# Performance work log

Hardware: AMD Instinct MI355X
Metric: run time of the kernel (lower is better)

The kernel has to match this reference:

```python
import jax, jax.numpy as jnp
import numpy as np

T, B, D, H = 2048, 64, 256, 512

def setup_inputs() -> dict:
    key = jax.random.key(0)
    ks = jax.random.split(key, 4)
    s = 1.0 / np.sqrt(D + H)  # nn.Linear default uniform scale approximated with normal*s
    return {
        "x": jax.random.normal(ks[0], (T, B, D), dtype=jnp.float32),
        "h0": jnp.zeros((B, H), dtype=jnp.float32),
        "Wz": jax.random.normal(ks[1], (D + H, H), dtype=jnp.float32) * s,
        "bz": jnp.zeros((H,), dtype=jnp.float32),
        "Wr": jax.random.normal(ks[2], (D + H, H), dtype=jnp.float32) * s,
        "br": jnp.zeros((H,), dtype=jnp.float32),
        "Wh": jax.random.normal(ks[3], (D + H, H), dtype=jnp.float32) * s,
        "bh": jnp.zeros((H,), dtype=jnp.float32),
    }

def reference(x, h0, Wz, bz, Wr, br, Wh, bh):
    """GRU over time: x [T,B,D], h0 [B,H]; returns hidden history [T,B,H]."""
    def step(h, xt):
        xh = jnp.concatenate([xt, h], axis=-1)          # [B, D+H]
        z = jax.nn.sigmoid(xh @ Wz + bz)                # update gate
        r = jax.nn.sigmoid(xh @ Wr + br)                # reset gate
        xrh = jnp.concatenate([xt, r * h], axis=-1)     # [B, D+H]
        h_tilde = jnp.tanh(xrh @ Wh + bh)               # candidate state
        h_new = (1.0 - z) * h + z * h_tilde
        return h_new, h_new
    _, hist = jax.lax.scan(step, h0, x)
    return hist
```

## Files before the change

### kernel.cpp

```cpp
#include <hip/hip_runtime.h>
#include <stdint.h>


#define T_STEPS 2048
#define B_SZ    64
#define D_SZ    256
#define H_SZ    512
#define NGROUP  4
#define NWG     64
#define MB      16

typedef __attribute__((ext_vector_type(8))) short  short8;
typedef __attribute__((ext_vector_type(4))) float  f32x4;
typedef unsigned long long u64;

__device__ __forceinline__ unsigned short f2bf(float v) {
  uint32_t u = __float_as_uint(v);
  return (unsigned short)((u + 0x7fffu + ((u >> 16) & 1u)) >> 16);
}
__device__ __forceinline__ float bf2f(unsigned short h) {
  return __uint_as_float(((uint32_t)h) << 16);
}
__device__ __forceinline__ void splitf(float v, short& hi, short& lo) {
  unsigned short h = f2bf(v);
  hi = (short)h;
  lo = (short)f2bf(v - bf2f(h));
}
__device__ __forceinline__ uint32_t packf(float v) {
  unsigned short h = f2bf(v);
  unsigned short l = f2bf(v - bf2f(h));
  return ((uint32_t)h << 16) | (uint32_t)l;
}
__device__ __forceinline__ float unpackf(uint32_t p) {
  return __uint_as_float(p & 0xffff0000u) + __uint_as_float(p << 16);
}

__device__ __forceinline__ uint32_t aload32(const uint32_t* p) {
  return __hip_atomic_load(p, __ATOMIC_RELAXED, __HIP_MEMORY_SCOPE_AGENT);
}
__device__ __forceinline__ u64 aload64(const uint32_t* p) {
  return __hip_atomic_load((const unsigned long long*)p, __ATOMIC_RELAXED,
                           __HIP_MEMORY_SCOPE_AGENT);
}
__device__ __forceinline__ void astore32(uint32_t* p, uint32_t v) {
  __hip_atomic_store(p, v, __ATOMIC_RELAXED, __HIP_MEMORY_SCOPE_AGENT);
}

__device__ __forceinline__ void lds_barrier() {
  asm volatile("s_waitcnt lgkmcnt(0)" ::: "memory");
  __builtin_amdgcn_s_barrier();
}

__device__ __forceinline__ void poll_flags(const uint32_t* fl, uint32_t tgt,
                                           int lane, int& cap) {
  int guard = 0;
  for (;;) {
    uint32_t v = aload32(fl + (lane & 31));
    if (__all((int)(v >= tgt))) break;
    if (++guard > cap) { cap = 256; break; }
    __builtin_amdgcn_s_sleep(1);
  }
}

__global__ void __launch_bounds__(256, 1)
gru_roles(const float* __restrict__ x, const float* __restrict__ h0,
          const float* __restrict__ Wz, const float* __restrict__ bz,
          const float* __restrict__ Wr, const float* __restrict__ br,
          const float* __restrict__ Wh, const float* __restrict__ bh,
          float* __restrict__ out,
          uint32_t* rh_flg, uint32_t* h_flg,
          uint32_t* h_pk, uint32_t* rh_pk, uint32_t* z_pk)
{
  __shared__ float partTa[16 * 64];
  __shared__ float partTb[16 * 64];

  const int tid  = threadIdx.x;
  const int wv   = tid >> 6;
  const int lane = tid & 63;
  const int blk  = blockIdx.x;
  const int g    = blk >> 6;
  const int wid  = blk & 63;
  const int m0   = g * MB;
  const bool isGate = (wid < 32);

  const int n     = lane & 15;
  const int kq    = lane >> 4;
  const int bfrag = m0 + n;
  const int m2    = kq * 4 + wv;
  const int n2    = n;
  const int b2    = m0 + m2;

  uint32_t* frh = rh_flg + g * 32;
  uint32_t* fh  = h_flg  + g * 32;

  int lch[6];
  lch[0] = 2 * wv; lch[1] = 2 * wv + 1;
  #pragma unroll
  for (int l = 2; l < 6; ++l) lch[l] = 8 + 4 * wv + (l - 2);

  int cap = 1 << 20;

  if (isGate) {
    const int c1  = wid * 16;
    const int col = c1 + n;

    short8 wzh[6], wzl[6], wrh_[6], wrl_[6];
    #pragma unroll
    for (int l = 0; l < 6; ++l) {
      #pragma unroll
      for (int j = 0; j < 8; ++j) {
        const int k = lch[l] * 32 + kq * 8 + j;
        short hi, lo;
        splitf(Wz[(size_t)k * H_SZ + col], hi, lo); wzh[l][j] = hi; wzl[l][j] = lo;
        splitf(Wr[(size_t)k * H_SZ + col], hi, lo); wrh_[l][j] = hi; wrl_[l][j] = lo;
      }
    }
    const float bzv = bz[col];
    const float brv = br[col];

    #pragma unroll 1
    for (int t = 0; t < T_STEPS; ++t) {
      f32x4 aZ = {0.f, 0.f, 0.f, 0.f};
      f32x4 aR = {0.f, 0.f, 0.f, 0.f};
      #pragma unroll
      for (int l = 0; l < 2; ++l) {
        const float* xp = x + ((size_t)t * B_SZ + bfrag) * D_SZ + lch[l] * 32 + kq * 8;
        float4 f0 = *(const float4*)xp;
        float4 f1 = *(const float4*)(xp + 4);
        float f[8] = {f0.x, f0.y, f0.z, f0.w, f1.x, f1.y, f1.z, f1.w};
        short8 xh, xl;
        #pragma unroll
        for (int j = 0; j < 8; ++j) { short hi, lo; splitf(f[j], hi, lo); xh[j] = hi; xl[j] = lo; }
        aZ = __builtin_amdgcn_mfma_f32_16x16x32_bf16(xh, wzh[l], aZ, 0, 0, 0);
        aZ = __builtin_amdgcn_mfma_f32_16x16x32_bf16(xl, wzh[l], aZ, 0, 0, 0);
        aZ = __builtin_amdgcn_mfma_f32_16x16x32_bf16(xh, wzl[l], aZ, 0, 0, 0);
        aR = __builtin_amdgcn_mfma_f32_16x16x32_bf16(xh, wrh_[l], aR, 0, 0, 0);
        aR = __builtin_amdgcn_mfma_f32_16x16x32_bf16(xl, wrh_[l], aR, 0, 0, 0);
        aR = __builtin_amdgcn_mfma_f32_16x16x32_bf16(xh, wrl_[l], aR, 0, 0, 0);
      }

      float hval;
      if (t > 0) {
        poll_flags(fh, (uint32_t)t, lane, cap);
        uint32_t hv = aload32(h_pk + (size_t)b2 * H_SZ + c1 + n2);
        #pragma unroll
        for (int l = 2; l < 6; ++l) {
          const int kh = (lch[l] - 8) * 32 + kq * 8;
          const uint32_t* hp = h_pk + (size_t)bfrag * H_SZ + kh;
          u64 q0 = aload64(hp),     q1 = aload64(hp + 2);
          u64 q2 = aload64(hp + 4), q3 = aload64(hp + 6);
          uint32_t u[8] = {(uint32_t)q0, (uint32_t)(q0 >> 32), (uint32_t)q1, (uint32_t)(q1 >> 32),
                           (uint32_t)q2, (uint32_t)(q2 >> 32), (uint32_t)q3, (uint32_t)(q3 >> 32)};
          short8 hh, hl;
          #pragma unroll
          for (int j = 0; j < 8; ++j) { hh[j] = (short)(u[j] >> 16); hl[j] = (short)(u[j] & 0xffffu); }
          aZ = __builtin_amdgcn_mfma_f32_16x16x32_bf16(hh, wzh[l], aZ, 0, 0, 0);
          aZ = __builtin_amdgcn_mfma_f32_16x16x32_bf16(hl, wzh[l], aZ, 0, 0, 0);
          aZ = __builtin_amdgcn_mfma_f32_16x16x32_bf16(hh, wzl[l], aZ, 0, 0, 0);
          aR = __builtin_amdgcn_mfma_f32_16x16x32_bf16(hh, wrh_[l], aR, 0, 0, 0);
          aR = __builtin_amdgcn_mfma_f32_16x16x32_bf16(hl, wrh_[l], aR, 0, 0, 0);
          aR = __builtin_amdgcn_mfma_f32_16x16x32_bf16(hh, wrl_[l], aR, 0, 0, 0);
        }
        hval = unpackf(hv);
      } else {
        hval = h0[(size_t)b2 * H_SZ + c1 + n2];
        #pragma unroll
        for (int l = 2; l < 6; ++l) {
          const int kh = (lch[l] - 8) * 32 + kq * 8;
          const float* hp = h0 + (size_t)bfrag * H_SZ + kh;
          float4 f0 = *(const float4*)hp;
          float4 f1 = *(const float4*)(hp + 4);
          float f[8] = {f0.x, f0.y, f0.z, f0.w, f1.x, f1.y, f1.z, f1.w};
          short8 hh, hl;
          #pragma unroll
          for (int j = 0; j < 8; ++j) { short hi, lo; splitf(f[j], hi, lo); hh[j] = hi; hl[j] = lo; }
          aZ = __builtin_amdgcn_mfma_f32_16x16x32_bf16(hh, wzh[l], aZ, 0, 0, 0);
          aZ = __builtin_amdgcn_mfma_f32_16x16x32_bf16(hl, wzh[l], aZ, 0, 0, 0);
          aZ = __builtin_amdgcn_mfma_f32_16x16x32_bf16(hh, wzl[l], aZ, 0, 0, 0);
          aR = __builtin_amdgcn_mfma_f32_16x16x32_bf16(hh, wrh_[l], aR, 0, 0, 0);
          aR = __builtin_amdgcn_mfma_f32_16x16x32_bf16(hl, wrh_[l], aR, 0, 0, 0);
          aR = __builtin_amdgcn_mfma_f32_16x16x32_bf16(hh, wrl_[l], aR, 0, 0, 0);
        }
      }

      #pragma unroll
      for (int r = 0; r < 4; ++r) {
        partTa[(wv * 4 + r) * 64 + lane] = aZ[r];
        partTb[(wv * 4 + r) * 64 + lane] = aR[r];
      }
      lds_barrier();
      {
        float sZ = partTa[(0 + wv) * 64 + lane] + partTa[(4 + wv) * 64 + lane]
                 + partTa[(8 + wv) * 64 + lane] + partTa[(12 + wv) * 64 + lane] + bzv;
        float sR = partTb[(0 + wv) * 64 + lane] + partTb[(4 + wv) * 64 + lane]
                 + partTb[(8 + wv) * 64 + lane] + partTb[(12 + wv) * 64 + lane] + brv;
        float zg = 1.f / (1.f + __expf(-sZ));
        float rg = 1.f / (1.f + __expf(-sR));
        astore32(z_pk  + (size_t)b2 * H_SZ + c1 + n2, __float_as_uint(zg));
        astore32(rh_pk + (size_t)b2 * H_SZ + c1 + n2, packf(rg * hval));
      }
      asm volatile("s_waitcnt vmcnt(0)" ::: "memory");
      lds_barrier();
      if (tid == 0) astore32(frh + wid, (uint32_t)(t + 1));
    }
  } else {
    const int c2  = (wid - 32) * 16;
    const int col = c2 + n;

    short8 whh_[6], whl_[6];
    #pragma unroll
    for (int l = 0; l < 6; ++l) {
      #pragma unroll
      for (int j = 0; j < 8; ++j) {
        const int k = lch[l] * 32 + kq * 8 + j;
        short hi, lo;
        splitf(Wh[(size_t)k * H_SZ + col], hi, lo); whh_[l][j] = hi; whl_[l][j] = lo;
      }
    }
    const float bhv = bh[col];

    float hreg = h0[(size_t)b2 * H_SZ + c2 + n2];

    #pragma unroll 1
    for (int t = 0; t < T_STEPS; ++t) {
      f32x4 acc = {0.f, 0.f, 0.f, 0.f};
      #pragma unroll
      for (int l = 0; l < 2; ++l) {
        const float* xp = x + ((size_t)t * B_SZ + bfrag) * D_SZ + lch[l] * 32 + kq * 8;
        float4 f0 = *(const float4*)xp;
        float4 f1 = *(const float4*)(xp + 4);
        float f[8] = {f0.x, f0.y, f0.z, f0.w, f1.x, f1.y, f1.z, f1.w};
        short8 xh, xl;
        #pragma unroll
        for (int j = 0; j < 8; ++j) { short hi, lo; splitf(f[j], hi, lo); xh[j] = hi; xl[j] = lo; }
        acc = __builtin_amdgcn_mfma_f32_16x16x32_bf16(xh, whh_[l], acc, 0, 0, 0);
        acc = __builtin_amdgcn_mfma_f32_16x16x32_bf16(xl, whh_[l], acc, 0, 0, 0);
        acc = __builtin_amdgcn_mfma_f32_16x16x32_bf16(xh, whl_[l], acc, 0, 0, 0);
      }

      poll_flags(frh, (uint32_t)(t + 1), lane, cap);
      uint32_t zu = aload32(z_pk + (size_t)b2 * H_SZ + c2 + n2);
      #pragma unroll
      for (int l = 2; l < 6; ++l) {
        const int kh = (lch[l] - 8) * 32 + kq * 8;
        const uint32_t* rp = rh_pk + (size_t)bfrag * H_SZ + kh;
        u64 q0 = aload64(rp),     q1 = aload64(rp + 2);
        u64 q2 = aload64(rp + 4), q3 = aload64(rp + 6);
        uint32_t u[8] = {(uint32_t)q0, (uint32_t)(q0 >> 32), (uint32_t)q1, (uint32_t)(q1 >> 32),
                         (uint32_t)q2, (uint32_t)(q2 >> 32), (uint32_t)q3, (uint32_t)(q3 >> 32)};
        short8 rh8, rl8;
        #pragma unroll
        for (int j = 0; j < 8; ++j) { rh8[j] = (short)(u[j] >> 16); rl8[j] = (short)(u[j] & 0xffffu); }
        acc = __builtin_amdgcn_mfma_f32_16x16x32_bf16(rh8, whh_[l], acc, 0, 0, 0);
        acc = __builtin_amdgcn_mfma_f32_16x16x32_bf16(rl8, whh_[l], acc, 0, 0, 0);
        acc = __builtin_amdgcn_mfma_f32_16x16x32_bf16(rh8, whl_[l], acc, 0, 0, 0);
      }

      #pragma unroll
      for (int r = 0; r < 4; ++r) partTa[(wv * 4 + r) * 64 + lane] = acc[r];
      lds_barrier();
      float hn;
      {
        float s = partTa[(0 + wv) * 64 + lane] + partTa[(4 + wv) * 64 + lane]
                + partTa[(8 + wv) * 64 + lane] + partTa[(12 + wv) * 64 + lane] + bhv;
        float e  = __expf(2.f * s);
        float ht = 1.f - 2.f / (e + 1.f);
        float zf = __uint_as_float(zu);
        hn = (1.f - zf) * hreg + zf * ht;
        hreg = hn;
        astore32(h_pk + (size_t)b2 * H_SZ + c2 + n2, packf(hn));
      }
      asm volatile("s_waitcnt vmcnt(0)" ::: "memory");
      lds_barrier();
      if (tid == 0) astore32(fh + (wid - 32), (uint32_t)(t + 1));

      __builtin_nontemporal_store(hn, out + ((size_t)t * B_SZ + b2) * H_SZ + c2 + n2);
    }
  }
}

extern "C" void kernel_launch(void* const* d_in, const int* in_sizes, int n_in,
                              void* d_out, int out_size, void* d_ws, size_t ws_size,
                              hipStream_t stream) {
  const float* x  = (const float*)d_in[0];
  const float* h0 = (const float*)d_in[1];
  const float* Wz = (const float*)d_in[2];
  const float* bz = (const float*)d_in[3];
  const float* Wr = (const float*)d_in[4];
  const float* br = (const float*)d_in[5];
  const float* Wh = (const float*)d_in[6];
  const float* bh = (const float*)d_in[7];
  float* out = (float*)d_out;

  char* ws = (char*)d_ws;
  uint32_t* rh_flg = (uint32_t*)(ws + 0);
  uint32_t* h_flg  = (uint32_t*)(ws + 2048);
  uint32_t* h_pk   = (uint32_t*)(ws + 8192);
  uint32_t* rh_pk  = (uint32_t*)(ws + 8192 + 131072);
  uint32_t* z_pk   = (uint32_t*)(ws + 8192 + 262144);

  hipMemsetAsync(d_ws, 0, 8192, stream);
  gru_roles<<<dim3(NGROUP * NWG), dim3(256), 0, stream>>>(
      x, h0, Wz, bz, Wr, br, Wh, bh, out,
      rh_flg, h_flg, h_pk, rh_pk, z_pk);
}
```

Before: 25.67 ms.

## Software-pipeline the input projection one step ahead of the recurrent dependency

The x-part of each gate's matmul is now computed for step t+1 while step t is finishing, and x for step t+2 is prefetched into registers after the flag store. This moves the x loads, the bf16 splitting and their MFMAs off the critical path between receiving h (or r*h) and publishing the next result. The cost is more live registers for the prefetch buffers and accumulators, and the prefetch loads are placed before the next step's vmcnt(0) wait.

```diff
diff --git a/kernel.cpp b/kernel.cpp
--- a/kernel.cpp
+++ b/kernel.cpp
@@ -118,27 +118,34 @@
     const float bzv = bz[col];
     const float brv = br[col];
 
+    f32x4 aZc = {0.f, 0.f, 0.f, 0.f};
+    f32x4 aRc = {0.f, 0.f, 0.f, 0.f};
+    float4 xb[2][2];
+    #pragma unroll
+    for (int l = 0; l < 2; ++l) {
+      const float* xp = x + (size_t)bfrag * D_SZ + lch[l] * 32 + kq * 8;
+      float4 f0 = *(const float4*)xp;
+      float4 f1 = *(const float4*)(xp + 4);
+      float f[8] = {f0.x, f0.y, f0.z, f0.w, f1.x, f1.y, f1.z, f1.w};
+      short8 xh, xl;
+      #pragma unroll
+      for (int j = 0; j < 8; ++j) { short hi, lo; splitf(f[j], hi, lo); xh[j] = hi; xl[j] = lo; }
+      aZc = __builtin_amdgcn_mfma_f32_16x16x32_bf16(xh, wzh[l], aZc, 0, 0, 0);
+      aZc = __builtin_amdgcn_mfma_f32_16x16x32_bf16(xl, wzh[l], aZc, 0, 0, 0);
+      aZc = __builtin_amdgcn_mfma_f32_16x16x32_bf16(xh, wzl[l], aZc, 0, 0, 0);
+      aRc = __builtin_amdgcn_mfma_f32_16x16x32_bf16(xh, wrh_[l], aRc, 0, 0, 0);
+      aRc = __builtin_amdgcn_mfma_f32_16x16x32_bf16(xl, wrh_[l], aRc, 0, 0, 0);
+      aRc = __builtin_amdgcn_mfma_f32_16x16x32_bf16(xh, wrl_[l], aRc, 0, 0, 0);
+    }
+    #pragma unroll
+    for (int l = 0; l < 2; ++l) {
+      const float* xp = x + ((size_t)1 * B_SZ + bfrag) * D_SZ + lch[l] * 32 + kq * 8;
+      xb[l][0] = *(const float4*)xp;
+      xb[l][1] = *(const float4*)(xp + 4);
+    }
+
     #pragma unroll 1
     for (int t = 0; t < T_STEPS; ++t) {
-      f32x4 aZ = {0.f, 0.f, 0.f, 0.f};
-      f32x4 aR = {0.f, 0.f, 0.f, 0.f};
-      #pragma unroll
-      for (int l = 0; l < 2; ++l) {
-        const float* xp = x + ((size_t)t * B_SZ + bfrag) * D_SZ + lch[l] * 32 + kq * 8;
-        float4 f0 = *(const float4*)xp;
-        float4 f1 = *(const float4*)(xp + 4);
-        float f[8] = {f0.x, f0.y, f0.z, f0.w, f1.x, f1.y, f1.z, f1.w};
-        short8 xh, xl;
-        #pragma unroll
-        for (int j = 0; j < 8; ++j) { short hi, lo; splitf(f[j], hi, lo); xh[j] = hi; xl[j] = lo; }
-        aZ = __builtin_amdgcn_mfma_f32_16x16x32_bf16(xh, wzh[l], aZ, 0, 0, 0);
-        aZ = __builtin_amdgcn_mfma_f32_16x16x32_bf16(xl, wzh[l], aZ, 0, 0, 0);
-        aZ = __builtin_amdgcn_mfma_f32_16x16x32_bf16(xh, wzl[l], aZ, 0, 0, 0);
-        aR = __builtin_amdgcn_mfma_f32_16x16x32_bf16(xh, wrh_[l], aR, 0, 0, 0);
-        aR = __builtin_amdgcn_mfma_f32_16x16x32_bf16(xl, wrh_[l], aR, 0, 0, 0);
-        aR = __builtin_amdgcn_mfma_f32_16x16x32_bf16(xh, wrl_[l], aR, 0, 0, 0);
-      }
-
       float hval;
       if (t > 0) {
         poll_flags(fh, (uint32_t)t, lane, cap);
@@ -154,12 +161,12 @@
           short8 hh, hl;
           #pragma unroll
           for (int j = 0; j < 8; ++j) { hh[j] = (short)(u[j] >> 16); hl[j] = (short)(u[j] & 0xffffu); }
-          aZ = __builtin_amdgcn_mfma_f32_16x16x32_bf16(hh, wzh[l], aZ, 0, 0, 0);
-          aZ = __builtin_amdgcn_mfma_f32_16x16x32_bf16(hl, wzh[l], aZ, 0, 0, 0);
-          aZ = __builtin_amdgcn_mfma_f32_16x16x32_bf16(hh, wzl[l], aZ, 0, 0, 0);
-          aR = __builtin_amdgcn_mfma_f32_16x16x32_bf16(hh, wrh_[l], aR, 0, 0, 0);
-          aR = __builtin_amdgcn_mfma_f32_16x16x32_bf16(hl, wrh_[l], aR, 0, 0, 0);
-          aR = __builtin_amdgcn_mfma_f32_16x16x32_bf16(hh, wrl_[l], aR, 0, 0, 0);
+          aZc = __builtin_amdgcn_mfma_f32_16x16x32_bf16(hh, wzh[l], aZc, 0, 0, 0);
+          aZc = __builtin_amdgcn_mfma_f32_16x16x32_bf16(hl, wzh[l], aZc, 0, 0, 0);
+          aZc = __builtin_amdgcn_mfma_f32_16x16x32_bf16(hh, wzl[l], aZc, 0, 0, 0);
+          aRc = __builtin_amdgcn_mfma_f32_16x16x32_bf16(hh, wrh_[l], aRc, 0, 0, 0);
+          aRc = __builtin_amdgcn_mfma_f32_16x16x32_bf16(hl, wrh_[l], aRc, 0, 0, 0);
+          aRc = __builtin_amdgcn_mfma_f32_16x16x32_bf16(hh, wrl_[l], aRc, 0, 0, 0);
         }
         hval = unpackf(hv);
       } else {
@@ -174,19 +181,19 @@
           short8 hh, hl;
           #pragma unroll
           for (int j = 0; j < 8; ++j) { short hi, lo; splitf(f[j], hi, lo); hh[j] = hi; hl[j] = lo; }
-          aZ = __builtin_amdgcn_mfma_f32_16x16x32_bf16(hh, wzh[l], aZ, 0, 0, 0);
-          aZ = __builtin_amdgcn_mfma_f32_16x16x32_bf16(hl, wzh[l], aZ, 0, 0, 0);
-          aZ = __builtin_amdgcn_mfma_f32_16x16x32_bf16(hh, wzl[l], aZ, 0, 0, 0);
-          aR = __builtin_amdgcn_mfma_f32_16x16x32_bf16(hh, wrh_[l], aR, 0, 0, 0);
-          aR = __builtin_amdgcn_mfma_f32_16x16x32_bf16(hl, wrh_[l], aR, 0, 0, 0);
-          aR = __builtin_amdgcn_mfma_f32_16x16x32_bf16(hh, wrl_[l], aR, 0, 0, 0);
+          aZc = __builtin_amdgcn_mfma_f32_16x16x32_bf16(hh, wzh[l], aZc, 0, 0, 0);
+          aZc = __builtin_amdgcn_mfma_f32_16x16x32_bf16(hl, wzh[l], aZc, 0, 0, 0);
+          aZc = __builtin_amdgcn_mfma_f32_16x16x32_bf16(hh, wzl[l], aZc, 0, 0, 0);
+          aRc = __builtin_amdgcn_mfma_f32_16x16x32_bf16(hh, wrh_[l], aRc, 0, 0, 0);
+          aRc = __builtin_amdgcn_mfma_f32_16x16x32_bf16(hl, wrh_[l], aRc, 0, 0, 0);
+          aRc = __builtin_amdgcn_mfma_f32_16x16x32_bf16(hh, wrl_[l], aRc, 0, 0, 0);
         }
       }
 
       #pragma unroll
       for (int r = 0; r < 4; ++r) {
-        partTa[(wv * 4 + r) * 64 + lane] = aZ[r];
-        partTb[(wv * 4 + r) * 64 + lane] = aR[r];
+        partTa[(wv * 4 + r) * 64 + lane] = aZc[r];
+        partTb[(wv * 4 + r) * 64 + lane] = aRc[r];
       }
       lds_barrier();
       {
@@ -199,9 +206,39 @@
         astore32(z_pk  + (size_t)b2 * H_SZ + c1 + n2, __float_as_uint(zg));
         astore32(rh_pk + (size_t)b2 * H_SZ + c1 + n2, packf(rg * hval));
       }
+
+      f32x4 aZn = {0.f, 0.f, 0.f, 0.f};
+      f32x4 aRn = {0.f, 0.f, 0.f, 0.f};
+      if (t + 1 < T_STEPS) {
+        #pragma unroll
+        for (int l = 0; l < 2; ++l) {
+          float f[8] = {xb[l][0].x, xb[l][0].y, xb[l][0].z, xb[l][0].w,
+                        xb[l][1].x, xb[l][1].y, xb[l][1].z, xb[l][1].w};
+          short8 xh, xl;
+          #pragma unroll
+          for (int j = 0; j < 8; ++j) { short hi, lo; splitf(f[j], hi, lo); xh[j] = hi; xl[j] = lo; }
+          aZn = __builtin_amdgcn_mfma_f32_16x16x32_bf16(xh, wzh[l], aZn, 0, 0, 0);
+          aZn = __builtin_amdgcn_mfma_f32_16x16x32_bf16(xl, wzh[l], aZn, 0, 0, 0);
+          aZn = __builtin_amdgcn_mfma_f32_16x16x32_bf16(xh, wzl[l], aZn, 0, 0, 0);
+          aRn = __builtin_amdgcn_mfma_f32_16x16x32_bf16(xh, wrh_[l], aRn, 0, 0, 0);
+          aRn = __builtin_amdgcn_mfma_f32_16x16x32_bf16(xl, wrh_[l], aRn, 0, 0, 0);
+          aRn = __builtin_amdgcn_mfma_f32_16x16x32_bf16(xh, wrl_[l], aRn, 0, 0, 0);
+        }
+      }
+
       asm volatile("s_waitcnt vmcnt(0)" ::: "memory");
       lds_barrier();
       if (tid == 0) astore32(frh + wid, (uint32_t)(t + 1));
+
+      if (t + 2 < T_STEPS) {
+        #pragma unroll
+        for (int l = 0; l < 2; ++l) {
+          const float* xp = x + ((size_t)(t + 2) * B_SZ + bfrag) * D_SZ + lch[l] * 32 + kq * 8;
+          xb[l][0] = *(const float4*)xp;
+          xb[l][1] = *(const float4*)(xp + 4);
+        }
+      }
+      aZc = aZn; aRc = aRn;
     }
   } else {
     const int c2  = (wid - 32) * 16;
@@ -221,23 +258,30 @@
 
     float hreg = h0[(size_t)b2 * H_SZ + c2 + n2];
 
+    f32x4 acc = {0.f, 0.f, 0.f, 0.f};
+    float4 xb[2][2];
+    #pragma unroll
+    for (int l = 0; l < 2; ++l) {
+      const float* xp = x + (size_t)bfrag * D_SZ + lch[l] * 32 + kq * 8;
+      float4 f0 = *(const float4*)xp;
+      float4 f1 = *(const float4*)(xp + 4);
+      float f[8] = {f0.x, f0.y, f0.z, f0.w, f1.x, f1.y, f1.z, f1.w};
+      short8 xh, xl;
+      #pragma unroll
+      for (int j = 0; j < 8; ++j) { short hi, lo; splitf(f[j], hi, lo); xh[j] = hi; xl[j] = lo; }
+      acc = __builtin_amdgcn_mfma_f32_16x16x32_bf16(xh, whh_[l], acc, 0, 0, 0);
+      acc = __builtin_amdgcn_mfma_f32_16x16x32_bf16(xl, whh_[l], acc, 0, 0, 0);
+      acc = __builtin_amdgcn_mfma_f32_16x16x32_bf16(xh, whl_[l], acc, 0, 0, 0);
+    }
+    #pragma unroll
+    for (int l = 0; l < 2; ++l) {
+      const float* xp = x + ((size_t)1 * B_SZ + bfrag) * D_SZ + lch[l] * 32 + kq * 8;
+      xb[l][0] = *(const float4*)xp;
+      xb[l][1] = *(const float4*)(xp + 4);
+    }
+
     #pragma unroll 1
     for (int t = 0; t < T_STEPS; ++t) {
-      f32x4 acc = {0.f, 0.f, 0.f, 0.f};
-      #pragma unroll
-      for (int l = 0; l < 2; ++l) {
-        const float* xp = x + ((size_t)t * B_SZ + bfrag) * D_SZ + lch[l] * 32 + kq * 8;
-        float4 f0 = *(const float4*)xp;
-        float4 f1 = *(const float4*)(xp + 4);
-        float f[8] = {f0.x, f0.y, f0.z, f0.w, f1.x, f1.y, f1.z, f1.w};
-        short8 xh, xl;
-        #pragma unroll
-        for (int j = 0; j < 8; ++j) { short hi, lo; splitf(f[j], hi, lo); xh[j] = hi; xl[j] = lo; }
-        acc = __builtin_amdgcn_mfma_f32_16x16x32_bf16(xh, whh_[l], acc, 0, 0, 0);
-        acc = __builtin_amdgcn_mfma_f32_16x16x32_bf16(xl, whh_[l], acc, 0, 0, 0);
-        acc = __builtin_amdgcn_mfma_f32_16x16x32_bf16(xh, whl_[l], acc, 0, 0, 0);
-      }
-
       poll_flags(frh, (uint32_t)(t + 1), lane, cap);
       uint32_t zu = aload32(z_pk + (size_t)b2 * H_SZ + c2 + n2);
       #pragma unroll
@@ -270,11 +314,36 @@
         hreg = hn;
         astore32(h_pk + (size_t)b2 * H_SZ + c2 + n2, packf(hn));
       }
+
+      f32x4 accn = {0.f, 0.f, 0.f, 0.f};
+      if (t + 1 < T_STEPS) {
+        #pragma unroll
+        for (int l = 0; l < 2; ++l) {
+          float f[8] = {xb[l][0].x, xb[l][0].y, xb[l][0].z, xb[l][0].w,
+                        xb[l][1].x, xb[l][1].y, xb[l][1].z, xb[l][1].w};
+          short8 xh, xl;
+          #pragma unroll
+          for (int j = 0; j < 8; ++j) { short hi, lo; splitf(f[j], hi, lo); xh[j] = hi; xl[j] = lo; }
+          accn = __builtin_amdgcn_mfma_f32_16x16x32_bf16(xh, whh_[l], accn, 0, 0, 0);
+          accn = __builtin_amdgcn_mfma_f32_16x16x32_bf16(xl, whh_[l], accn, 0, 0, 0);
+          accn = __builtin_amdgcn_mfma_f32_16x16x32_bf16(xh, whl_[l], accn, 0, 0, 0);
+        }
+      }
+
       asm volatile("s_waitcnt vmcnt(0)" ::: "memory");
       lds_barrier();
       if (tid == 0) astore32(fh + (wid - 32), (uint32_t)(t + 1));
 
+      if (t + 2 < T_STEPS) {
+        #pragma unroll
+        for (int l = 0; l < 2; ++l) {
+          const float* xp = x + ((size_t)(t + 2) * B_SZ + bfrag) * D_SZ + lch[l] * 32 + kq * 8;
+          xb[l][0] = *(const float4*)xp;
+          xb[l][1] = *(const float4*)(xp + 4);
+        }
+      }
       __builtin_nontemporal_store(hn, out + ((size_t)t * B_SZ + b2) * H_SZ + c2 + n2);
+      acc = accn;
     }
   }
 }
```

New measurement: 25.41 ms. About the same (-1.0%).
